# Kernel optimization log

Measured on AMD Instinct MI355X. Metric: run time of the kernel, lower is better.

The kernel has to match this reference:

```python
import jax, jax.numpy as jnp
import numpy as np
import math

# ---- config (mirrors FastRCNNRoIHeads init args) ----
B, N, C = 8, 2048, 2            # images, proposals/img, classes (incl. background)
K = 100                          # detections_per_img
IMG_H, IMG_W = 512, 512
SCORE_THRESH = 0.05
NMS_THRESH = 0.4
MIN_SIZE = 0.01
WX, WY, WW, WH = 10.0, 10.0, 5.0, 5.0   # BoxCoder weights
BBOX_XFORM_CLIP = math.log(1000.0 / 16.0)


def setup_inputs() -> dict:
    key = jax.random.key(0)
    k1, k2, k3, k4, k5 = jax.random.split(key, 5)
    prop_clss = jax.random.normal(k1, (B, N, C), dtype=jnp.float32)
    prop_regs = 0.1 * jax.random.normal(k2, (B, N, 4), dtype=jnp.float32)
    prop_qlts = jax.random.normal(k3, (B, N, 1), dtype=jnp.float32)
    # valid proposal boxes inside the image: x1,y1 in [0,448), w,h in [16,128)
    xy1 = jax.random.uniform(k4, (B, N, 2), dtype=jnp.float32) * 380.0
    wh = 16.0 + jax.random.uniform(k5, (B, N, 2), dtype=jnp.float32) * 112.0
    props = jnp.concatenate([xy1, xy1 + wh], axis=-1)
    return {"prop_clss": prop_clss, "prop_regs": prop_regs,
            "prop_qlts": prop_qlts, "props": props}


def _decode(regs, props):
    # torchvision BoxCoder.decode_single, class-agnostic [N,4] deltas
    w = props[:, 2] - props[:, 0]
    h = props[:, 3] - props[:, 1]
    cx = props[:, 0] + 0.5 * w
    cy = props[:, 1] + 0.5 * h
    dx, dy = regs[:, 0] / WX, regs[:, 1] / WY
    dw = jnp.minimum(regs[:, 2] / WW, BBOX_XFORM_CLIP)
    dh = jnp.minimum(regs[:, 3] / WH, BBOX_XFORM_CLIP)
    pcx, pcy = dx * w + cx, dy * h + cy
    pw, ph = jnp.exp(dw) * w, jnp.exp(dh) * h
    return jnp.stack([pcx - 0.5 * pw, pcy - 0.5 * ph,
                      pcx + 0.5 * pw, pcy + 0.5 * ph], axis=-1)


def _iou_matrix(b):
    area = (b[:, 2] - b[:, 0]) * (b[:, 3] - b[:, 1])
    lt = jnp.maximum(b[:, None, :2], b[None, :, :2])
    rb = jnp.minimum(b[:, None, 2:], b[None, :, 2:])
    wh = jnp.clip(rb - lt, 0.0)
    inter = wh[..., 0] * wh[..., 1]
    return inter / (area[:, None] + area[None, :] - inter + 1e-9)


def _postprocess_one(clss, regs, qlts, props):
    boxes = _decode(regs, props)
    boxes = jnp.stack([jnp.clip(boxes[:, 0], 0.0, IMG_W),
                       jnp.clip(boxes[:, 1], 0.0, IMG_H),
                       jnp.clip(boxes[:, 2], 0.0, IMG_W),
                       jnp.clip(boxes[:, 3], 0.0, IMG_H)], axis=-1)
    small_ok = ((boxes[:, 2] - boxes[:, 0]) >= MIN_SIZE) & \
               ((boxes[:, 3] - boxes[:, 1]) >= MIN_SIZE)
    raw = jax.nn.softmax(clss, axis=-1)[:, 1:]          # [N, C-1]
    q = jax.nn.sigmoid(qlts[:, 0])                      # [N]
    scores = (q[:, None] * raw).reshape(-1)             # [N*(C-1)]
    raw_f = raw.reshape(-1)
    Cm1 = C - 1
    M = N * Cm1
    prop_idx = jnp.arange(M) // Cm1
    cls_idx = jnp.arange(M) % Cm1 + 1
    valid = (raw_f > SCORE_THRESH) & small_ok[prop_idx]
    cand_boxes = boxes[prop_idx]                        # [M,4]
    # batched_nms: offset boxes per class so NMS runs per class
    max_coord = jnp.max(cand_boxes)
    boxes_off = cand_boxes + (cls_idx.astype(boxes.dtype) * (max_coord + 1.0))[:, None]
    masked = jnp.where(valid, scores, -1.0)
    order = jnp.argsort(-masked)
    b_s = cand_boxes[order]
    bo_s = boxes_off[order]
    s_s = scores[order]
    c_s = cls_idx[order]
    v_s = valid[order]
    iou = _iou_matrix(bo_s)                             # [M,M]
    idxs = jnp.arange(M)

    def step(keep, i):
        sup = (iou[i] > NMS_THRESH) & (idxs > i)
        keep = jnp.where(keep[i], keep & ~sup, keep)
        return keep, None

    keep, _ = jax.lax.scan(step, v_s, idxs)
    rank = jnp.cumsum(keep.astype(jnp.int32)) - 1
    dest = jnp.where(keep & (rank < K), rank, K)        # K = dump slot
    out_b = jnp.zeros((K + 1, 4), boxes.dtype).at[dest].set(b_s)[:K]
    out_s = jnp.zeros((K + 1,), boxes.dtype).at[dest].set(s_s)[:K]
    out_c = jnp.zeros((K + 1,), jnp.int32).at[dest].set(c_s.astype(jnp.int32))[:K]
    return out_b, out_s, out_c


def reference(prop_clss, prop_regs, prop_qlts, props):
    boxes, scores, classes = jax.vmap(_postprocess_one)(
        prop_clss, prop_regs, prop_qlts, props)
    return boxes, scores, classes
```

## Files before the change

kernel.cpp:

```cpp
#include <hip/hip_runtime.h>
#include <stdint.h>

#define NPROP 2048
#define NCLS  2
#define KDET  100
#define BT    512
#define NMS_TH 0.4f

__device__ __forceinline__ float dec_score(uint64_t k) {
    uint32_t u = ~(uint32_t)(k >> 32);
    uint32_t bits = (u & 0x80000000u) ? (u & 0x7FFFFFFFu) : ~u;
    return __uint_as_float(bits);
}

__device__ __forceinline__ float bcastf(float v, int srclane) {
    return __uint_as_float((uint32_t)__builtin_amdgcn_readlane(__float_as_int(v), srclane));
}

__device__ __forceinline__ void decode_one(
    const float* __restrict__ clss, const float* __restrict__ regs,
    const float* __restrict__ qlts, const float* __restrict__ props,
    int b, int i, float4& boxOut, uint64_t& keyOut, float& mxOut)
{
    const float CLIPV = 4.135166556742356f;
    float4 p  = ((const float4*)props)[b * NPROP + i];
    float4 rg = ((const float4*)regs)[b * NPROP + i];
    float2 cc = ((const float2*)clss)[b * NPROP + i];
    float  qv = qlts[(size_t)b * NPROP + i];

    float w  = __fsub_rn(p.z, p.x);
    float h  = __fsub_rn(p.w, p.y);
    float cx = __fadd_rn(p.x, __fmul_rn(0.5f, w));
    float cy = __fadd_rn(p.y, __fmul_rn(0.5f, h));
    float dx = __fdiv_rn(rg.x, 10.0f);
    float dy = __fdiv_rn(rg.y, 10.0f);
    float dw = fminf(__fdiv_rn(rg.z, 5.0f), CLIPV);
    float dh = fminf(__fdiv_rn(rg.w, 5.0f), CLIPV);
    float pcx = __fadd_rn(__fmul_rn(dx, w), cx);
    float pcy = __fadd_rn(__fmul_rn(dy, h), cy);
    float pw  = __fmul_rn(expf(dw), w);
    float ph  = __fmul_rn(expf(dh), h);
    float x1 = __fsub_rn(pcx, __fmul_rn(0.5f, pw));
    float y1 = __fsub_rn(pcy, __fmul_rn(0.5f, ph));
    float x2 = __fadd_rn(pcx, __fmul_rn(0.5f, pw));
    float y2 = __fadd_rn(pcy, __fmul_rn(0.5f, ph));
    x1 = fminf(fmaxf(x1, 0.0f), 512.0f);
    y1 = fminf(fmaxf(y1, 0.0f), 512.0f);
    x2 = fminf(fmaxf(x2, 0.0f), 512.0f);
    y2 = fminf(fmaxf(y2, 0.0f), 512.0f);
    bool small_ok = (__fsub_rn(x2, x1) >= 0.01f) && (__fsub_rn(y2, y1) >= 0.01f);

    float m  = fmaxf(cc.x, cc.y);
    float e0 = expf(__fsub_rn(cc.x, m));
    float e1 = expf(__fsub_rn(cc.y, m));
    float raw = __fdiv_rn(e1, __fadd_rn(e0, e1));
    float sq  = __fdiv_rn(1.0f, __fadd_rn(1.0f, expf(-qv)));
    float score = __fmul_rn(sq, raw);
    bool valid = (raw > 0.05f) && small_ok;
    float masked = valid ? score : -1.0f;

    boxOut = make_float4(x1, y1, x2, y2);
    uint32_t fb = __float_as_uint(masked);
    uint32_t u  = (fb & 0x80000000u) ? ~fb : (fb | 0x80000000u);
    keyOut = ((uint64_t)(~u) << 32) | (uint32_t)i;
    mxOut = fmaxf(fmaxf(x1, y1), fmaxf(x2, y2));
}

__device__ __forceinline__ void bitonic2048(uint64_t key[4], uint64_t* skey,
                                            int idxBase, int lane)
{
    for (int k = 2; k <= NPROP; k <<= 1) {
        for (int j = k >> 1; j > 0; j >>= 1) {
            if (j >= 256) {
                __syncthreads();
#pragma unroll
                for (int r = 0; r < 4; ++r) {
                    int idx = idxBase + r;
                    skey[(idx >> 2) | ((idx & 3) << 9)] = key[r];
                }
                __syncthreads();
#pragma unroll
                for (int r = 0; r < 4; ++r) {
                    int idx  = idxBase + r;
                    int pidx = idx ^ j;
                    uint64_t o = skey[(pidx >> 2) | ((pidx & 3) << 9)];
                    bool takeMin = (((idx & k) == 0) == ((idx & j) == 0));
                    bool lt = key[r] < o;
                    uint64_t mn = lt ? key[r] : o, mx = lt ? o : key[r];
                    key[r] = takeMin ? mn : mx;
                }
            } else if (j >= 4) {
                int lx = j >> 2;
#pragma unroll
                for (int r = 0; r < 4; ++r) {
                    int idx = idxBase + r;
                    uint64_t o = __shfl_xor(key[r], lx, 64);
                    bool takeMin = (((idx & k) == 0) == ((lane & lx) == 0));
                    bool lt = key[r] < o;
                    uint64_t mn = lt ? key[r] : o, mx = lt ? o : key[r];
                    key[r] = takeMin ? mn : mx;
                }
            } else {
#pragma unroll
                for (int r = 0; r < 4; ++r) {
                    if ((r & j) == 0) {
                        int rh = r | j;
                        int idx = idxBase + r;
                        bool up = ((idx & k) == 0);
                        uint64_t a = key[r], c2 = key[rh];
                        bool lt = a < c2;
                        uint64_t mn = lt ? a : c2, mx = lt ? c2 : a;
                        key[r] = up ? mn : mx; key[rh] = up ? mx : mn;
                    }
                }
            }
        }
    }
}

__global__ __launch_bounds__(BT) void PRISM_71511205479155_kernel(
    const float* __restrict__ clss, const float* __restrict__ regs,
    const float* __restrict__ qlts, const float* __restrict__ props,
    float* __restrict__ out, int B)
{
    __shared__ float4   sbox[NPROP];
    __shared__ uint64_t skey[NPROP];
    __shared__ uint64_t s_colpart[8 * 64];
    __shared__ uint64_t s_inpart[8];
    __shared__ float4   s_kbox[KDET];
    __shared__ float    s_karea[KDET];
    __shared__ int      s_keep[KDET];
    __shared__ int      s_maxc, s_kept, s_nvalid;

    const int b = blockIdx.x, tid = threadIdx.x, lane = tid & 63, wv = tid >> 6;
    const int idxBase = (wv << 8) | (lane << 2);

    if (tid == 0) { s_maxc = 0; s_kept = 0; s_nvalid = NPROP; }
    __syncthreads();

    uint64_t key[4];
    float thmax = 0.0f;
#pragma unroll
    for (int r = 0; r < 4; ++r) {
        int i = idxBase + r;
        float4 bx; uint64_t k; float mx;
        decode_one(clss, regs, qlts, props, b, i, bx, k, mx);
        sbox[i] = bx; key[r] = k;
        thmax = fmaxf(thmax, mx);
    }
#pragma unroll
    for (int d = 1; d < 64; d <<= 1) thmax = fmaxf(thmax, __shfl_xor(thmax, d, 64));
    if (lane == 0) atomicMax(&s_maxc, __float_as_int(thmax));

    bitonic2048(key, skey, idxBase, lane);

    __syncthreads();
#pragma unroll
    for (int r = 0; r < 4; ++r) skey[idxBase + r] = key[r];
    {
        int fi = 4;
#pragma unroll
        for (int r = 3; r >= 0; --r) if ((key[r] >> 63) != 0) fi = r;
        uint64_t anyb = __ballot(fi < 4);
        if (anyb) {
            int L = (int)__builtin_ctzll(anyb);
            int fiL = __shfl(fi, L, 64);
            if (lane == 0) atomicMin(&s_nvalid, (wv << 8) + (L << 2) + fiL);
        }
    }
    __syncthreads();

    const float off = __fadd_rn(__int_as_float(s_maxc), 1.0f);
    const int nv = s_nvalid;

    int c = 0;
    while (true) {
        __syncthreads();
        int kept = s_kept;
        if (c >= nv || kept >= KDET) break;
        int W = min(64, nv - c);
        bool have = (lane < W);

        float qx1 = 0.f, qy1 = 0.f, qx2 = 0.f, qy2 = 0.f, qa = 0.f;
        if (have) {
            float4 bx = sbox[(uint32_t)skey[c + lane]];
            qx1 = __fadd_rn(bx.x, off); qy1 = __fadd_rn(bx.y, off);
            qx2 = __fadd_rn(bx.z, off); qy2 = __fadd_rn(bx.w, off);
            qa  = __fmul_rn(__fsub_rn(qx2, qx1), __fsub_rn(qy2, qy1));
        }

        uint64_t colpart = 0;
#pragma unroll
        for (int t = 0; t < 8; ++t) {
            int i = wv + (t << 3);
            bool rowok = (i < W);
            int isrc = rowok ? i : 0;
            float rx1 = bcastf(qx1, isrc);
            float ry1 = bcastf(qy1, isrc);
            float rx2 = bcastf(qx2, isrc);
            float ry2 = bcastf(qy2, isrc);
            float ra  = bcastf(qa , isrc);
            float ltx = fmaxf(rx1, qx1), lty = fmaxf(ry1, qy1);
            float rbx = fminf(rx2, qx2), rby = fminf(ry2, qy2);
            float iw = fmaxf(__fsub_rn(rbx, ltx), 0.0f);
            float ih = fmaxf(__fsub_rn(rby, lty), 0.0f);
            float inter = __fmul_rn(iw, ih);
            float denom = __fadd_rn(__fsub_rn(__fadd_rn(ra, qa), inter), 1e-9f);
            float iou   = __fdiv_rn(inter, denom);
            bool pred = rowok && have && (lane > i) && (iou > NMS_TH);
            uint64_t bm = (uint64_t)__ballot(pred);
            colpart |= ((bm >> lane) & 1ull) << isrc;
        }
        s_colpart[(wv << 6) | lane] = colpart;

        bool supin = false;
        if (have && kept) {
            for (int ki = wv; ki < kept; ki += 8) {
                float4 ko = s_kbox[ki];
                float  ka = s_karea[ki];
                float ltx = fmaxf(ko.x, qx1), lty = fmaxf(ko.y, qy1);
                float rbx = fminf(ko.z, qx2), rby = fminf(ko.w, qy2);
                float iw = fmaxf(__fsub_rn(rbx, ltx), 0.0f);
                float ih = fmaxf(__fsub_rn(rby, lty), 0.0f);
                float inter = __fmul_rn(iw, ih);
                float denom = __fadd_rn(__fsub_rn(__fadd_rn(ka, qa), inter), 1e-9f);
                supin = supin || (__fdiv_rn(inter, denom) > NMS_TH);
            }
        }
        uint64_t inb = (uint64_t)__ballot(supin);
        if (lane == 0) s_inpart[wv] = inb;
        __syncthreads();

        if (wv == 0) {
            uint64_t col = 0, insup = 0;
#pragma unroll
            for (int w2 = 0; w2 < 8; ++w2) {
                col   |= s_colpart[(w2 << 6) | lane];
                insup |= s_inpart[w2];
            }
            bool aliveBit = have && !((insup >> lane) & 1ull);
            uint64_t keepM = (uint64_t)__ballot(aliveBit);
            for (int it = 0; it < 64; ++it) {
                uint64_t nk = (uint64_t)__ballot(aliveBit && ((col & keepM) == 0ull));
                if (nk == keepM) break;
                keepM = nk;
            }
            int quota = KDET - kept;
            int nNew  = __popcll(keepM);
            int take  = nNew < quota ? nNew : quota;
            uint64_t below = keepM & ~(~0ull << lane);
            int rank = __popcll(below);
            bool mine = (((keepM >> lane) & 1ull) != 0ull) && (rank < quota);
            if (mine) {
                s_keep[kept + rank]  = c + lane;
                s_kbox[kept + rank]  = make_float4(qx1, qy1, qx2, qy2);
                s_karea[kept + rank] = qa;
            }
            if (lane == 0) s_kept = kept + take;
        }
        c += 64;
    }
    __syncthreads();

    float* out_boxes  = out;
    float* out_scores = out + (size_t)B * KDET * 4;
    float* out_cls    = out + (size_t)B * KDET * 5;
    int kept = s_kept;
    for (int s = tid; s < KDET; s += BT) {
        float* ob = out_boxes + ((size_t)b * KDET + s) * 4;
        if (s < kept) {
            uint64_t kk = skey[s_keep[s]];
            float4 bx = sbox[(uint32_t)kk];
            ob[0] = bx.x; ob[1] = bx.y; ob[2] = bx.z; ob[3] = bx.w;
            out_scores[(size_t)b * KDET + s] = dec_score(kk);
            out_cls[(size_t)b * KDET + s]    = 1.0f;
        } else {
            ob[0] = 0.0f; ob[1] = 0.0f; ob[2] = 0.0f; ob[3] = 0.0f;
            out_scores[(size_t)b * KDET + s] = 0.0f;
            out_cls[(size_t)b * KDET + s]    = 0.0f;
        }
    }
}

extern "C" void kernel_launch(void* const* d_in, const int* in_sizes, int n_in,
                              void* d_out, int out_size, void* d_ws, size_t ws_size,
                              hipStream_t stream) {
    const float* clss  = (const float*)d_in[0];
    const float* regs  = (const float*)d_in[1];
    const float* qlts  = (const float*)d_in[2];
    const float* props = (const float*)d_in[3];
    float* out = (float*)d_out;

    int B = in_sizes[0] / (NPROP * NCLS);

    PRISM_71511205479155_kernel<<<B, BT, 0, stream>>>(clss, regs, qlts, props, out, B);
}
```

Measured before the change: 40.59 us.

## Select top candidates via histogram before sorting, fall back to full bitonic sort

Builds a shared-memory histogram over the top bits of each sort key to find a bucket threshold that covers roughly the best 256 valid candidates. Only those candidates (at most 512) are compacted and sorted by a single wavefront, and NMS runs over this reduced list. If that pass keeps fewer than 100 boxes while more valid candidates exist, or the threshold bucket overflows, it redoes the full 2048-element bitonic sort and NMS. This avoids the full block-wide sort in the common case, at the cost of extra histogram and scan work and a slower fallback path.

```diff
diff --git a/kernel.cpp b/kernel.cpp
--- a/kernel.cpp
+++ b/kernel.cpp
@@ -118,72 +118,22 @@
     }
 }
 
-__global__ __launch_bounds__(BT) void PRISM_71511205479155_kernel(
-    const float* __restrict__ clss, const float* __restrict__ regs,
-    const float* __restrict__ qlts, const float* __restrict__ props,
-    float* __restrict__ out, int B)
+__device__ __forceinline__ int phaseC(
+    const uint64_t* keys, int nv, const float4* sboxp, float off,
+    uint64_t* s_colpart, uint64_t* s_inpart, float4* s_kbox, float* s_karea,
+    int* s_keep, int* s_kept, int lane, int wv)
 {
-    __shared__ float4   sbox[NPROP];
-    __shared__ uint64_t skey[NPROP];
-    __shared__ uint64_t s_colpart[8 * 64];
-    __shared__ uint64_t s_inpart[8];
-    __shared__ float4   s_kbox[KDET];
-    __shared__ float    s_karea[KDET];
-    __shared__ int      s_keep[KDET];
-    __shared__ int      s_maxc, s_kept, s_nvalid;
-
-    const int b = blockIdx.x, tid = threadIdx.x, lane = tid & 63, wv = tid >> 6;
-    const int idxBase = (wv << 8) | (lane << 2);
-
-    if (tid == 0) { s_maxc = 0; s_kept = 0; s_nvalid = NPROP; }
-    __syncthreads();
-
-    uint64_t key[4];
-    float thmax = 0.0f;
-#pragma unroll
-    for (int r = 0; r < 4; ++r) {
-        int i = idxBase + r;
-        float4 bx; uint64_t k; float mx;
-        decode_one(clss, regs, qlts, props, b, i, bx, k, mx);
-        sbox[i] = bx; key[r] = k;
-        thmax = fmaxf(thmax, mx);
-    }
-#pragma unroll
-    for (int d = 1; d < 64; d <<= 1) thmax = fmaxf(thmax, __shfl_xor(thmax, d, 64));
-    if (lane == 0) atomicMax(&s_maxc, __float_as_int(thmax));
-
-    bitonic2048(key, skey, idxBase, lane);
-
-    __syncthreads();
-#pragma unroll
-    for (int r = 0; r < 4; ++r) skey[idxBase + r] = key[r];
-    {
-        int fi = 4;
-#pragma unroll
-        for (int r = 3; r >= 0; --r) if ((key[r] >> 63) != 0) fi = r;
-        uint64_t anyb = __ballot(fi < 4);
-        if (anyb) {
-            int L = (int)__builtin_ctzll(anyb);
-            int fiL = __shfl(fi, L, 64);
-            if (lane == 0) atomicMin(&s_nvalid, (wv << 8) + (L << 2) + fiL);
-        }
-    }
-    __syncthreads();
-
-    const float off = __fadd_rn(__int_as_float(s_maxc), 1.0f);
-    const int nv = s_nvalid;
-
     int c = 0;
     while (true) {
         __syncthreads();
-        int kept = s_kept;
+        int kept = *s_kept;
         if (c >= nv || kept >= KDET) break;
         int W = min(64, nv - c);
         bool have = (lane < W);
 
         float qx1 = 0.f, qy1 = 0.f, qx2 = 0.f, qy2 = 0.f, qa = 0.f;
         if (have) {
-            float4 bx = sbox[(uint32_t)skey[c + lane]];
+            float4 bx = sboxp[(uint32_t)keys[c + lane]];
             qx1 = __fadd_rn(bx.x, off); qy1 = __fadd_rn(bx.y, off);
             qx2 = __fadd_rn(bx.z, off); qy2 = __fadd_rn(bx.w, off);
             qa  = __fmul_rn(__fsub_rn(qx2, qx1), __fsub_rn(qy2, qy1));
@@ -256,20 +206,170 @@
                 s_kbox[kept + rank]  = make_float4(qx1, qy1, qx2, qy2);
                 s_karea[kept + rank] = qa;
             }
-            if (lane == 0) s_kept = kept + take;
+            if (lane == 0) *s_kept = kept + take;
         }
         c += 64;
     }
     __syncthreads();
+    return *s_kept;
+}
+
+__global__ __launch_bounds__(BT) void PRISM_71511205479155_kernel(
+    const float* __restrict__ clss, const float* __restrict__ regs,
+    const float* __restrict__ qlts, const float* __restrict__ props,
+    float* __restrict__ out, int B)
+{
+    __shared__ float4   sbox[NPROP];
+    __shared__ uint64_t skey[NPROP];
+    __shared__ uint64_t cand[512];
+    __shared__ uint32_t hist[1024];
+    __shared__ uint64_t s_colpart[8 * 64];
+    __shared__ uint64_t s_inpart[8];
+    __shared__ float4   s_kbox[KDET];
+    __shared__ float    s_karea[KDET];
+    __shared__ int      s_keep[KDET];
+    __shared__ int      s_wsum[8];
+    __shared__ int      s_maxc, s_kept, s_beta, s_M, s_totV, s_cnt, s_fb;
+
+    const int b = blockIdx.x, tid = threadIdx.x, lane = tid & 63, wv = tid >> 6;
+    const int idxBase = (wv << 8) | (lane << 2);
+
+    hist[tid] = 0; hist[tid + 512] = 0;
+    cand[tid] = ~0ull;
+    if (tid == 0) { s_maxc = 0; s_kept = 0; s_beta = -1; s_M = 0; s_totV = 0; s_cnt = 0; s_fb = 0; }
+    __syncthreads();
+
+    uint64_t key[4];
+    float thmax = 0.0f;
+#pragma unroll
+    for (int r = 0; r < 4; ++r) {
+        int i = idxBase + r;
+        float4 bx; uint64_t k; float mx;
+        decode_one(clss, regs, qlts, props, b, i, bx, k, mx);
+        sbox[i] = bx; skey[i] = k; key[r] = k;
+        thmax = fmaxf(thmax, mx);
+        uint32_t bkt = (uint32_t)(k >> 53);
+        if (bkt < 1024)
+            atomicAdd(&hist[bkt >> 1], (bkt & 1) ? 0x10000u : 1u);
+    }
+#pragma unroll
+    for (int d = 1; d < 64; d <<= 1) thmax = fmaxf(thmax, __shfl_xor(thmax, d, 64));
+    if (lane == 0) atomicMax(&s_maxc, __float_as_int(thmax));
+    __syncthreads();
+
+    {
+        uint32_t w0 = hist[2 * tid], w1 = hist[2 * tid + 1];
+        uint32_t c0 = w0 & 0xFFFFu, c1 = w0 >> 16, c2 = w1 & 0xFFFFu, c3 = w1 >> 16;
+        uint32_t local = c0 + c1 + c2 + c3;
+        uint32_t incl = local;
+#pragma unroll
+        for (int d = 1; d < 64; d <<= 1) {
+            uint32_t v = __shfl_up(incl, d, 64);
+            if (lane >= d) incl += v;
+        }
+        if (lane == 63) s_wsum[wv] = (int)incl;
+        __syncthreads();
+        int base = 0, tot = 0;
+#pragma unroll
+        for (int w = 0; w < 8; ++w) {
+            int sv = s_wsum[w];
+            tot += sv;
+            if (w < wv) base += sv;
+        }
+        int target = tot < 256 ? tot : 256;
+        uint32_t run = (uint32_t)base + incl - local;
+        uint32_t cc[4] = {c0, c1, c2, c3};
+#pragma unroll
+        for (int r = 0; r < 4; ++r) {
+            uint32_t ci = run + cc[r];
+            if (target > 0 && (int)run < target && (int)ci >= target) {
+                s_beta = 4 * tid + r;
+                s_M = (int)ci;
+                if (ci > 512) s_fb = 1;
+            }
+            run = ci;
+        }
+        if (tid == 0) s_totV = tot;
+        __syncthreads();
+    }
+
+    const float off = __fadd_rn(__int_as_float(s_maxc), 1.0f);
+    const int beta = s_beta, M = s_M, totV = s_totV;
+    int fb = s_fb;
+
+    if (!fb) {
+#pragma unroll
+        for (int r = 0; r < 4; ++r) {
+            if ((int)(key[r] >> 53) <= beta) {
+                int p = atomicAdd(&s_cnt, 1);
+                cand[p] = key[r];
+            }
+        }
+        __syncthreads();
+
+        if (wv == 0) {
+            uint64_t q[8];
+#pragma unroll
+            for (int r = 0; r < 8; ++r) q[r] = cand[(lane << 3) | r];
+            for (int k2 = 2; k2 <= 512; k2 <<= 1) {
+                for (int j = k2 >> 1; j > 0; j >>= 1) {
+                    if (j >= 8) {
+                        int lx = j >> 3;
+#pragma unroll
+                        for (int r = 0; r < 8; ++r) {
+                            int idx = (lane << 3) | r;
+                            uint64_t o = __shfl_xor(q[r], lx, 64);
+                            bool takeMin = (((idx & k2) == 0) == ((idx & j) == 0));
+                            bool lt = q[r] < o;
+                            uint64_t mn = lt ? q[r] : o, mx = lt ? o : q[r];
+                            q[r] = takeMin ? mn : mx;
+                        }
+                    } else {
+#pragma unroll
+                        for (int r = 0; r < 8; ++r) {
+                            if ((r & j) == 0) {
+                                int rh = r | j;
+                                int idx = (lane << 3) | r;
+                                bool up = ((idx & k2) == 0);
+                                uint64_t a = q[r], c2 = q[rh];
+                                bool lt = a < c2;
+                                uint64_t mn = lt ? a : c2, mx = lt ? c2 : a;
+                                q[r] = up ? mn : mx; q[rh] = up ? mx : mn;
+                            }
+                        }
+                    }
+                }
+            }
+#pragma unroll
+            for (int r = 0; r < 8; ++r) cand[(lane << 3) | r] = q[r];
+        }
+        __syncthreads();
+    }
+
+    int kept = 0;
+    if (!fb) kept = phaseC(cand, M, sbox, off, s_colpart, s_inpart,
+                           s_kbox, s_karea, s_keep, &s_kept, lane, wv);
+
+    bool needFull = fb || (kept < KDET && M < totV);
+    if (needFull) {
+        if (tid == 0) s_kept = 0;
+        bitonic2048(key, skey, idxBase, lane);
+        __syncthreads();
+#pragma unroll
+        for (int r = 0; r < 4; ++r) skey[idxBase + r] = key[r];
+        __syncthreads();
+        kept = phaseC(skey, totV, sbox, off, s_colpart, s_inpart,
+                      s_kbox, s_karea, s_keep, &s_kept, lane, wv);
+    }
+    const uint64_t* fkeys = needFull ? skey : cand;
 
     float* out_boxes  = out;
     float* out_scores = out + (size_t)B * KDET * 4;
     float* out_cls    = out + (size_t)B * KDET * 5;
-    int kept = s_kept;
     for (int s = tid; s < KDET; s += BT) {
         float* ob = out_boxes + ((size_t)b * KDET + s) * 4;
         if (s < kept) {
-            uint64_t kk = skey[s_keep[s]];
+            uint64_t kk = fkeys[s_keep[s]];
             float4 bx = sbox[(uint32_t)kk];
             ob[0] = bx.x; ob[1] = bx.y; ob[2] = bx.z; ob[3] = bx.w;
             out_scores[(size_t)b * KDET + s] = dec_score(kk);
```

After: 39.75 us. 1.02x faster.
